# Performance work log

Measured on AMD Instinct MI355X. Metric: run time of the kernel, lower is better.

The kernel has to match this reference:

```python
import jax, jax.numpy as jnp
import numpy as np

BETA = 0.25  # init kwarg; exercises the 0 <= beta < 1 loss branch


def setup_inputs() -> dict:
    key = jax.random.key(0)
    k1, k2 = jax.random.split(key)
    N, D, K = 65536, 64, 4096
    x = jax.random.normal(k1, (N, D), dtype=jnp.float32)
    # original: uniform(-1/K, 1/K) then mean-centered; exact init distribution
    codebook = jax.random.uniform(k2, (K, D), dtype=jnp.float32,
                                  minval=-1.0 / K, maxval=1.0 / K)
    codebook = codebook - codebook.mean(axis=0, keepdims=True)
    return {"x": x, "codebook": codebook}


def reference(x, codebook):
    # pairwise squared distances via sum-of-squares + matmul: [N, K]
    dist = (jnp.sum(x * x, axis=1, keepdims=True)
            + jnp.sum(codebook * codebook, axis=1)
            - 2.0 * jnp.matmul(x, codebook.T))
    encoding_inds = jnp.argmin(dist, axis=1)            # [N]
    # gather codebook rows (equivalent to one-hot @ codebook, no one-hot materialized)
    quantized = jnp.take(codebook, encoding_inds, axis=0)  # [N, D]
    # straight-through estimator
    x_quantized = x + jax.lax.stop_gradient(quantized - x)
    mse = lambda a, b: jnp.mean((a - b) ** 2)
    loss = (BETA * mse(x, jax.lax.stop_gradient(quantized))
            + mse(quantized, jax.lax.stop_gradient(x)))
    return x_quantized, encoding_inds[:, None], loss
```

## Files before the change

kernel.cpp:

```cpp
#include <hip/hip_runtime.h>


#define D  64
#define NT 256

typedef unsigned short u16;
typedef short bf16x8 __attribute__((ext_vector_type(8)));
typedef float f32x4  __attribute__((ext_vector_type(4)));

#define VMWAIT_(n) asm volatile("s_waitcnt vmcnt(" #n ")" ::: "memory")
#define VMWAIT(n) VMWAIT_(n)

__device__ __forceinline__ u16 f32_to_bf16_raw(float f) {
    union { float f; unsigned u; } v; v.f = f;
    unsigned u = v.u;
    u += 0x7FFFu + ((u >> 16) & 1u);
    return (u16)(u >> 16);
}
__device__ __forceinline__ float bf16_raw_to_f32(u16 h) {
    union { unsigned u; float f; } v; v.u = ((unsigned)h) << 16;
    return v.f;
}
__device__ __forceinline__ f32x4 mfma16(bf16x8 a, bf16x8 b, f32x4 c) {
    return __builtin_amdgcn_mfma_f32_16x16x32_bf16(a, b, c, 0, 0, 0);
}

__device__ __forceinline__ float np_pairwise_sumsq_64(const float* p) {
    float r[8];
    #pragma unroll
    for (int j = 0; j < 8; ++j) r[j] = __fmul_rn(p[j], p[j]);
    #pragma unroll
    for (int i = 8; i < 64; i += 8) {
        #pragma unroll
        for (int j = 0; j < 8; ++j)
            r[j] = __fadd_rn(r[j], __fmul_rn(p[i + j], p[i + j]));
    }
    float t0 = __fadd_rn(r[0], r[1]);
    float t1 = __fadd_rn(r[2], r[3]);
    float t2 = __fadd_rn(r[4], r[5]);
    float t3 = __fadd_rn(r[6], r[7]);
    return __fadd_rn(__fadd_rn(t0, t1), __fadd_rn(t2, t3));
}

__global__ __launch_bounds__(256) void prep_kernel(const float* __restrict__ x,
                                                   const float* __restrict__ cb,
                                                   float* __restrict__ sx,
                                                   float* __restrict__ sc,
                                                   bf16x8* __restrict__ cbf,
                                                   int* __restrict__ amb_cnt) {
    int b = blockIdx.x;
    if (b == 0 && threadIdx.x == 0) *amb_cnt = 0;
    if (b < 272) {
        const float* a = (b < 256) ? x : cb;
        float* o = (b < 256) ? sx : sc;
        int r0 = (b < 256) ? b * 256 : (b - 256) * 256;
        int r = r0 + threadIdx.x;
        float buf[64];
        const float4* p = (const float4*)(a + (size_t)r * D);
        #pragma unroll
        for (int i = 0; i < 16; ++i) {
            float4 v = p[i];
            buf[4*i] = v.x; buf[4*i+1] = v.y; buf[4*i+2] = v.z; buf[4*i+3] = v.w;
        }
        o[r] = np_pairwise_sumsq_64(buf);
    } else {
        int t = b - 272;
        int tid = threadIdx.x;
        int lane = tid & 63;
        int ks = (tid >> 6) & 1;
        int hl = tid >> 7;
        int code = t * 16 + (lane & 15);
        int g = lane >> 4;
        bf16x8 v;
        #pragma unroll
        for (int j = 0; j < 8; ++j) {
            int d = ks * 32 + g * 4 + (j & 3) + 16 * (j >> 2);
            float val = cb[(size_t)code * D + d];
            u16 h = f32_to_bf16_raw(val);
            if (hl) {
                float resid = val - bf16_raw_to_f32(h);
                h = f32_to_bf16_raw(resid);
            }
            v[j] = (short)h;
        }
        cbf[((size_t)t * 4 + hl * 2 + ks) * 64 + lane] = v;
    }
}

#define MARG_A 8.0e-6f
#define MARG_B 5.0e-7f

#define STAGE(T, BUF) do {                                                    \
    const char* _src = (const char*)cbf + (size_t)(T) * 4096 + lane * 16;     \
    char* _dst = ringbase + (BUF) * 4096 + lane * 16;                         \
    __builtin_amdgcn_global_load_lds((const __attribute__((address_space(1))) unsigned int*)(_src),        (__attribute__((address_space(3))) unsigned int*)(_dst),        16, 0, 0); \
    __builtin_amdgcn_global_load_lds((const __attribute__((address_space(1))) unsigned int*)(_src + 1024), (__attribute__((address_space(3))) unsigned int*)(_dst + 1024), 16, 0, 0); \
    __builtin_amdgcn_global_load_lds((const __attribute__((address_space(1))) unsigned int*)(_src + 2048), (__attribute__((address_space(3))) unsigned int*)(_dst + 2048), 16, 0, 0); \
    __builtin_amdgcn_global_load_lds((const __attribute__((address_space(1))) unsigned int*)(_src + 3072), (__attribute__((address_space(3))) unsigned int*)(_dst + 3072), 16, 0, 0); \
} while (0)

#define DSREAD(T, BUF, SCK) do {                                              \
    const bf16x8* _bfr = (const bf16x8*)(ringbase + (BUF) * 4096);            \
    Fb0h = _bfr[lane]; Fb1h = _bfr[64 + lane];                                \
    Fb0l = _bfr[128 + lane]; Fb1l = _bfr[192 + lane];                         \
    SCK = scl[(T) * 16 + r];                                                  \
} while (0)

#define MFMAC(P) do {                                                         \
    _Pragma("unroll")                                                         \
    for (int s = 0; s < 4; ++s) {                                             \
        f32x4 _a = {0.f, 0.f, 0.f, 0.f};                                      \
        _a = mfma16(Ah0[s], Fb0h, _a);                                        \
        _a = mfma16(Ah1[s], Fb1h, _a);                                        \
        _a = mfma16(Ah0[s], Fb0l, _a);                                        \
        _a = mfma16(Ah1[s], Fb1l, _a);                                        \
        _a = mfma16(Al0[s], Fb0h, _a);                                        \
        _a = mfma16(Al1[s], Fb1h, _a);                                        \
        P[s] = _a;                                                            \
    }                                                                         \
} while (0)

#define VALUU(P, SCK, T) do {                                                 \
    int _kc = (T) * 16 + r;                                                   \
    _Pragma("unroll")                                                         \
    for (int s = 0; s < 4; ++s) {                                             \
        _Pragma("unroll")                                                     \
        for (int q = 0; q < 4; ++q) {                                         \
            int u = s * 4 + q;                                                \
            float sv = __fmaf_rn(-2.0f, P[s][q], __fadd_rn(sxr[u], SCK));     \
            m2[u] = fminf(m2[u], fmaxf(m1[u], sv));                           \
            bool lt = sv < m1[u];                                             \
            i1[u] = lt ? _kc : i1[u];                                         \
            m1[u] = fminf(m1[u], sv);                                         \
        }                                                                     \
    }                                                                         \
} while (0)

#define ITF(I, BR, BS, PA, PB, SA, SB) do {                                   \
    VMWAIT(4);                                                                \
    DSREAD(t0 + (I) + 2, BR, SB);                                             \
    STAGE(t0 + (I) + 4, BS);                                                  \
    VALUU(PA, SA, t0 + (I));                                                  \
    MFMAC(PB);                                                                \
} while (0)
#define ITN(I, BR, PA, PB, SA, SB, WN) do {                                   \
    VMWAIT(WN);                                                               \
    DSREAD(t0 + (I) + 2, BR, SB);                                             \
    VALUU(PA, SA, t0 + (I));                                                  \
    MFMAC(PB);                                                                \
} while (0)
#define ITV(I, PA, SA) do { VALUU(PA, SA, t0 + (I)); } while (0)

__global__ __launch_bounds__(256, 2) void phase1_kernel(
    const float* __restrict__ x, const float* __restrict__ sx,
    const float* __restrict__ sc, const bf16x8* __restrict__ cbf,
    int* __restrict__ idxbuf, int* __restrict__ amb_cnt, int* __restrict__ amb_rows)
{
    __shared__ __align__(16) char ring[4][3][4096];
    __shared__ float scl[4096];
    __shared__ float lm1[128][2], lm2[128][2];
    __shared__ int   li1[128][2];

    const int tid  = threadIdx.x;
    const int w    = tid >> 6;
    const int lane = tid & 63;
    const int r = lane & 15, g = lane >> 4;
    const int half = w & 1;
    const int rowg = w >> 1;
    const int wbase = blockIdx.x * 128 + rowg * 64;

    for (int j = tid; j < 1024; j += 256)
        *(float4*)&scl[j * 4] = *(const float4*)&sc[j * 4];
    __syncthreads();

    bf16x8 Ah0[4], Ah1[4], Al0[4], Al1[4];
    #pragma unroll
    for (int s = 0; s < 4; ++s) {
        const float* xr = x + (size_t)(wbase + s * 16 + r) * D;
        float e0[8], e1[8];
        float4 f0 = *(const float4*)(xr + g * 4);
        float4 f1 = *(const float4*)(xr + 16 + g * 4);
        float4 f2 = *(const float4*)(xr + 32 + g * 4);
        float4 f3 = *(const float4*)(xr + 48 + g * 4);
        e0[0]=f0.x;e0[1]=f0.y;e0[2]=f0.z;e0[3]=f0.w; e0[4]=f1.x;e0[5]=f1.y;e0[6]=f1.z;e0[7]=f1.w;
        e1[0]=f2.x;e1[1]=f2.y;e1[2]=f2.z;e1[3]=f2.w; e1[4]=f3.x;e1[5]=f3.y;e1[6]=f3.z;e1[7]=f3.w;
        #pragma unroll
        for (int j = 0; j < 8; ++j) {
            u16 h0 = f32_to_bf16_raw(e0[j]);
            Ah0[s][j] = (short)h0;
            Al0[s][j] = (short)f32_to_bf16_raw(e0[j] - bf16_raw_to_f32(h0));
            u16 h1 = f32_to_bf16_raw(e1[j]);
            Ah1[s][j] = (short)h1;
            Al1[s][j] = (short)f32_to_bf16_raw(e1[j] - bf16_raw_to_f32(h1));
        }
    }

    float sxr[16], m1[16], m2[16];
    int   i1[16];
    #pragma unroll
    for (int u = 0; u < 16; ++u) {
        sxr[u] = sx[wbase + (u >> 2) * 16 + g * 4 + (u & 3)];
        m1[u] = 3.4e38f; m2[u] = 3.4e38f; i1[u] = 0;
    }

    const int t0 = half * 128;
    char* ringbase = &ring[w][0][0];

    bf16x8 Fb0h, Fb1h, Fb0l, Fb1l;
    f32x4  P0[4], P1[4], P2[4];
    float  sck0, sck1, sck2;

    VMWAIT(0);
    STAGE(t0 + 0, 0); STAGE(t0 + 1, 1);
    VMWAIT(4); DSREAD(t0 + 0, 0, sck0); STAGE(t0 + 2, 2); MFMAC(P0);
    VMWAIT(4); DSREAD(t0 + 1, 1, sck1); STAGE(t0 + 3, 0); MFMAC(P1);

    #pragma unroll 1
    for (int i = 0; i < 120; i += 3) {
        ITF(i + 0, 2, 1, P0, P2, sck0, sck2);
        ITF(i + 1, 0, 2, P1, P0, sck1, sck0);
        ITF(i + 2, 1, 0, P2, P1, sck2, sck1);
    }
    ITF(120, 2, 1, P0, P2, sck0, sck2);
    ITF(121, 0, 2, P1, P0, sck1, sck0);
    ITF(122, 1, 0, P2, P1, sck2, sck1);
    ITF(123, 2, 1, P0, P2, sck0, sck2);
    ITN(124, 0, P1, P0, sck1, sck0, 4);
    ITN(125, 1, P2, P1, sck2, sck1, 0);
    ITV(126, P0, sck0);
    ITV(127, P1, sck1);

    #pragma unroll
    for (int u = 0; u < 16; ++u) {
        #pragma unroll
        for (int mm = 1; mm < 16; mm <<= 1) {
            float om1 = __shfl_xor(m1[u], mm, 64);
            float om2 = __shfl_xor(m2[u], mm, 64);
            int   oi1 = __shfl_xor(i1[u], mm, 64);
            float nm2 = fminf(fmaxf(m1[u], om1), fminf(m2[u], om2));
            i1[u] = (om1 < m1[u]) ? oi1 : i1[u];
            m1[u] = fminf(m1[u], om1);
            m2[u] = nm2;
        }
    }
    if (r == 0) {
        #pragma unroll
        for (int u = 0; u < 16; ++u) {
            int rowin = rowg * 64 + (u >> 2) * 16 + g * 4 + (u & 3);
            lm1[rowin][half] = m1[u];
            lm2[rowin][half] = m2[u];
            li1[rowin][half] = i1[u];
        }
    }
    __syncthreads();

    if (tid < 128) {
        float a1 = lm1[tid][0], b1 = lm1[tid][1];
        float a2 = lm2[tid][0], b2 = lm2[tid][1];
        int   ia = li1[tid][0], ib = li1[tid][1];
        float m1f = fminf(a1, b1);
        float m2f = fminf(fmaxf(a1, b1), fminf(a2, b2));
        int   i1f = (b1 < a1) ? ib : ia;
        int orow = blockIdx.x * 128 + tid;
        idxbuf[orow] = i1f;
        float marg = __fmaf_rn(sx[orow], MARG_B, MARG_A);
        if (m2f - m1f <= marg) {
            int slot = atomicAdd(amb_cnt, 1);
            amb_rows[slot] = orow;
        }
    }
}

__global__ __launch_bounds__(256) void exact_scan(
    const float* __restrict__ x, const float* __restrict__ cb,
    const float* __restrict__ sx, const float* __restrict__ sc,
    const int* __restrict__ amb_cnt, const int* __restrict__ amb_rows,
    int* __restrict__ idxbuf)
{
    __shared__ float csT[4][64][64];
    __shared__ float xsT[64][16];
    __shared__ float redv[16][64];
    __shared__ int   redi[16][64];
    __shared__ float sxl[16];
    __shared__ int   rowids[16];

    const int tid = threadIdx.x;
    const int cnt = *amb_cnt;
    const int tz = tid >> 6, ty = (tid >> 4) & 3, cx = tid & 15;

    for (int base = blockIdx.x * 16; base < cnt; base += gridDim.x * 16) {
        if (tid < 16) {
            int i = base + tid;
            int rr = (i < cnt) ? amb_rows[i] : amb_rows[base];
            rowids[tid] = rr;
            sxl[tid] = sx[rr];
        }
        __syncthreads();
        {
            int rr = rowids[tid >> 4];
            int dg = tid & 15;
            float4 v = *(const float4*)(x + (size_t)rr * D + dg * 4);
            xsT[dg*4+0][tid>>4] = v.x; xsT[dg*4+1][tid>>4] = v.y;
            xsT[dg*4+2][tid>>4] = v.z; xsT[dg*4+3][tid>>4] = v.w;
        }

        float bv[4]; int bi[4];
        #pragma unroll
        for (int i = 0; i < 4; ++i) { bv[i] = 3.4e38f; bi[i] = 0x7fffffff; }

        for (int st = 0; st < 16; ++st) {
            __syncthreads();
            {
                int code = st * 256 + tid;
                const float4* src = (const float4*)(cb + (size_t)code * D);
                #pragma unroll
                for (int dd = 0; dd < 16; ++dd) {
                    float4 v = src[dd];
                    csT[tid>>6][dd*4+0][tid&63] = v.x; csT[tid>>6][dd*4+1][tid&63] = v.y;
                    csT[tid>>6][dd*4+2][tid&63] = v.z; csT[tid>>6][dd*4+3][tid&63] = v.w;
                }
            }
            __syncthreads();

            float acc[4][4];
            #pragma unroll
            for (int i = 0; i < 4; ++i)
                #pragma unroll
                for (int j = 0; j < 4; ++j) acc[i][j] = 0.0f;

            #pragma unroll 4
            for (int d = 0; d < 64; ++d) {
                float4 xv = *(const float4*)&xsT[d][ty * 4];
                float4 cv = *(const float4*)&csT[tz][d][cx * 4];
                float xr[4] = {xv.x, xv.y, xv.z, xv.w};
                float cc[4] = {cv.x, cv.y, cv.z, cv.w};
                #pragma unroll
                for (int i = 0; i < 4; ++i)
                    #pragma unroll
                    for (int j = 0; j < 4; ++j)
                        acc[i][j] = __fmaf_rn(xr[i], cc[j], acc[i][j]);
            }
            #pragma unroll
            for (int j = 0; j < 4; ++j) {
                int k = st * 256 + tz * 64 + cx * 4 + j;
                float sck = sc[k];
                #pragma unroll
                for (int i = 0; i < 4; ++i) {
                    float tt = __fadd_rn(sxl[ty * 4 + i], sck);
                    float u  = __fmul_rn(2.0f, acc[i][j]);
                    float s  = __fsub_rn(tt, u);
                    if (s < bv[i] || (s == bv[i] && k < bi[i])) { bv[i] = s; bi[i] = k; }
                }
            }
        }

        #pragma unroll
        for (int i = 0; i < 4; ++i) { redv[ty*4+i][tz*16+cx] = bv[i]; redi[ty*4+i][tz*16+cx] = bi[i]; }
        __syncthreads();
        if (tid < 16) {
            float bvv = redv[tid][0]; int bii = redi[tid][0];
            #pragma unroll 8
            for (int i = 1; i < 64; ++i) {
                float v = redv[tid][i]; int k = redi[tid][i];
                if (v < bvv || (v == bvv && k < bii)) { bvv = v; bii = k; }
            }
            idxbuf[rowids[tid]] = bii;
        }
        __syncthreads();
    }
}

__global__ __launch_bounds__(256) void finalize_rows(
    const float* __restrict__ x, const float* __restrict__ cb,
    const int* __restrict__ idxbuf,
    float* __restrict__ out_q, float* __restrict__ out_i,
    double* __restrict__ partials, int N)
{
    __shared__ double wsum[4];
    int wid = threadIdx.x >> 6, lane = threadIdx.x & 63;
    int n = blockIdx.x * 4 + wid;

    int idx = idxbuf[n];
    float q  = cb[(size_t)idx * D + lane];
    float xv = x[(size_t)n * D + lane];
    out_q[(size_t)n * D + lane] = q;

    double diff = (double)xv - (double)q;
    double s = diff * diff;
    #pragma unroll
    for (int off = 32; off > 0; off >>= 1) s += __shfl_down(s, off, 64);
    if (lane == 0) { wsum[wid] = s; out_i[n] = (float)idx; }
    __syncthreads();
    if (threadIdx.x == 0) partials[blockIdx.x] = (wsum[0] + wsum[1]) + (wsum[2] + wsum[3]);
}

__global__ __launch_bounds__(256) void loss_kernel(const double* __restrict__ partials,
                                                   int nP, float* __restrict__ out_loss,
                                                   double invND)
{
    __shared__ double red[256];
    double s = 0.0;
    for (int i = threadIdx.x; i < nP; i += 256) s += partials[i];
    red[threadIdx.x] = s;
    __syncthreads();
    #pragma unroll
    for (int step = 128; step > 0; step >>= 1) {
        if ((int)threadIdx.x < step) red[threadIdx.x] += red[threadIdx.x + step];
        __syncthreads();
    }
    if (threadIdx.x == 0) {
        double m = red[0] * invND;
        out_loss[0] = (float)(0.25 * m + m);
    }
}

extern "C" void kernel_launch(void* const* d_in, const int* in_sizes, int n_in,
                              void* d_out, int out_size, void* d_ws, size_t ws_size,
                              hipStream_t stream)
{
    const float* x  = (const float*)d_in[0];
    const float* cb = (const float*)d_in[1];
    const int N = in_sizes[0] / D;
    const int K = in_sizes[1] / D;

    float* out      = (float*)d_out;
    float* out_q    = out;
    float* out_i    = out + (size_t)N * D;
    float* out_loss = out_i + N;

    char* ws = (char*)d_ws;
    bf16x8* cbf      = (bf16x8*)ws;
    size_t off = (size_t)(K / 16) * 4 * 64 * sizeof(bf16x8);
    float*  sx       = (float*)(ws + off);  off += (size_t)N * 4;
    float*  sc       = (float*)(ws + off);  off += (size_t)K * 4;
    int*    idxbuf   = (int*)(ws + off);    off += (size_t)N * 4;
    int*    amb_rows = (int*)(ws + off);    off += (size_t)N * 4;
    double* partials = (double*)(ws + off); off += (size_t)(N / 4) * 8;
    int*    amb_cnt  = (int*)(ws + off);

    prep_kernel<<<272 + K / 16, 256, 0, stream>>>(x, cb, sx, sc, cbf, amb_cnt);
    phase1_kernel<<<N / 128, 256, 0, stream>>>(x, sx, sc, cbf, idxbuf, amb_cnt, amb_rows);
    exact_scan<<<1024, 256, 0, stream>>>(x, cb, sx, sc, amb_cnt, amb_rows, idxbuf);
    finalize_rows<<<N / 4, 256, 0, stream>>>(x, cb, idxbuf, out_q, out_i, partials, N);
    loss_kernel<<<1, 256, 0, stream>>>(partials, N / 4, out_loss,
                                       1.0 / ((double)N * (double)D));
}
```

Before: 244.3 us.

## Rework phase1 pipeline, drop row-norm term, fuse loss reduction via atomics

The phase1 loop now uses two accumulator sets with a three-slot LDS ring and one-tile lookahead instead of three, and drops the occupancy-2 launch bound. The per-row norm is removed from the inner comparison, since it is constant per row and argmin does not depend on it. The min/second-min update now uses fmed3, and the ambiguity margins are widened to match. The separate loss kernel is replaced by double atomics plus a last-block-done counter inside a grid-strided finalize kernel. This saves a launch and VALU work, but atomics add contention and shallower prefetch may expose latency.

```diff
diff --git a/kernel.cpp b/kernel.cpp
--- a/kernel.cpp
+++ b/kernel.cpp
@@ -47,9 +47,11 @@
                                                    float* __restrict__ sx,
                                                    float* __restrict__ sc,
                                                    bf16x8* __restrict__ cbf,
-                                                   int* __restrict__ amb_cnt) {
+                                                   int* __restrict__ amb_cnt,
+                                                   double* __restrict__ loss_acc,
+                                                   int* __restrict__ done_cnt) {
     int b = blockIdx.x;
-    if (b == 0 && threadIdx.x == 0) *amb_cnt = 0;
+    if (b == 0 && threadIdx.x == 0) { *amb_cnt = 0; *loss_acc = 0.0; *done_cnt = 0; }
     if (b < 272) {
         const float* a = (b < 256) ? x : cb;
         float* o = (b < 256) ? sx : sc;
@@ -87,8 +89,8 @@
     }
 }
 
-#define MARG_A 8.0e-6f
-#define MARG_B 5.0e-7f
+#define MARG_A 1.6e-5f
+#define MARG_B 6.5e-7f
 
 #define STAGE(T, BUF) do {                                                    \
     const char* _src = (const char*)cbf + (size_t)(T) * 4096 + lane * 16;     \
@@ -127,31 +129,24 @@
         _Pragma("unroll")                                                     \
         for (int q = 0; q < 4; ++q) {                                         \
             int u = s * 4 + q;                                                \
-            float sv = __fmaf_rn(-2.0f, P[s][q], __fadd_rn(sxr[u], SCK));     \
-            m2[u] = fminf(m2[u], fmaxf(m1[u], sv));                           \
-            bool lt = sv < m1[u];                                             \
-            i1[u] = lt ? _kc : i1[u];                                         \
-            m1[u] = fminf(m1[u], sv);                                         \
+            float sv = __fmaf_rn(-2.0f, P[s][q], SCK);                        \
+            float m1o = m1[u];                                                \
+            m2[u] = __builtin_amdgcn_fmed3f(sv, m1o, m2[u]);                  \
+            i1[u] = (sv < m1o) ? _kc : i1[u];                                 \
+            m1[u] = fminf(m1o, sv);                                           \
         }                                                                     \
     }                                                                         \
 } while (0)
 
-#define ITF(I, BR, BS, PA, PB, SA, SB) do {                                   \
+#define ITX(I, Pv, Sv, Pm, Sm, BR, BS) do {                                   \
     VMWAIT(4);                                                                \
-    DSREAD(t0 + (I) + 2, BR, SB);                                             \
-    STAGE(t0 + (I) + 4, BS);                                                  \
-    VALUU(PA, SA, t0 + (I));                                                  \
-    MFMAC(PB);                                                                \
+    DSREAD(t0 + (I) + 1, BR, Sm);                                             \
+    STAGE(t0 + (I) + 3, BS);                                                  \
+    VALUU(Pv, Sv, t0 + (I));                                                  \
+    MFMAC(Pm);                                                                \
 } while (0)
-#define ITN(I, BR, PA, PB, SA, SB, WN) do {                                   \
-    VMWAIT(WN);                                                               \
-    DSREAD(t0 + (I) + 2, BR, SB);                                             \
-    VALUU(PA, SA, t0 + (I));                                                  \
-    MFMAC(PB);                                                                \
-} while (0)
-#define ITV(I, PA, SA) do { VALUU(PA, SA, t0 + (I)); } while (0)
-
-__global__ __launch_bounds__(256, 2) void phase1_kernel(
+
+__global__ __launch_bounds__(256) void phase1_kernel(
     const float* __restrict__ x, const float* __restrict__ sx,
     const float* __restrict__ sc, const bf16x8* __restrict__ cbf,
     int* __restrict__ idxbuf, int* __restrict__ amb_cnt, int* __restrict__ amb_rows)
@@ -195,40 +190,41 @@
         }
     }
 
-    float sxr[16], m1[16], m2[16];
+    float m1[16], m2[16];
     int   i1[16];
     #pragma unroll
-    for (int u = 0; u < 16; ++u) {
-        sxr[u] = sx[wbase + (u >> 2) * 16 + g * 4 + (u & 3)];
-        m1[u] = 3.4e38f; m2[u] = 3.4e38f; i1[u] = 0;
-    }
+    for (int u = 0; u < 16; ++u) { m1[u] = 3.4e38f; m2[u] = 3.4e38f; i1[u] = 0; }
 
     const int t0 = half * 128;
     char* ringbase = &ring[w][0][0];
 
     bf16x8 Fb0h, Fb1h, Fb0l, Fb1l;
-    f32x4  P0[4], P1[4], P2[4];
-    float  sck0, sck1, sck2;
+    f32x4  PA[4], PB[4];
+    float  sA, sB;
 
     VMWAIT(0);
-    STAGE(t0 + 0, 0); STAGE(t0 + 1, 1);
-    VMWAIT(4); DSREAD(t0 + 0, 0, sck0); STAGE(t0 + 2, 2); MFMAC(P0);
-    VMWAIT(4); DSREAD(t0 + 1, 1, sck1); STAGE(t0 + 3, 0); MFMAC(P1);
+    STAGE(t0 + 0, 0); STAGE(t0 + 1, 1); STAGE(t0 + 2, 2);
+    VMWAIT(8);
+    DSREAD(t0 + 0, 0, sA);
+    MFMAC(PA);
 
     #pragma unroll 1
-    for (int i = 0; i < 120; i += 3) {
-        ITF(i + 0, 2, 1, P0, P2, sck0, sck2);
-        ITF(i + 1, 0, 2, P1, P0, sck1, sck0);
-        ITF(i + 2, 1, 0, P2, P1, sck2, sck1);
-    }
-    ITF(120, 2, 1, P0, P2, sck0, sck2);
-    ITF(121, 0, 2, P1, P0, sck1, sck0);
-    ITF(122, 1, 0, P2, P1, sck2, sck1);
-    ITF(123, 2, 1, P0, P2, sck0, sck2);
-    ITN(124, 0, P1, P0, sck1, sck0, 4);
-    ITN(125, 1, P2, P1, sck2, sck1, 0);
-    ITV(126, P0, sck0);
-    ITV(127, P1, sck1);
+    for (int i = 0; i < 120; i += 6) {
+        ITX(i + 0, PA, sA, PB, sB, 1, 0);
+        ITX(i + 1, PB, sB, PA, sA, 2, 1);
+        ITX(i + 2, PA, sA, PB, sB, 0, 2);
+        ITX(i + 3, PB, sB, PA, sA, 1, 0);
+        ITX(i + 4, PA, sA, PB, sB, 2, 1);
+        ITX(i + 5, PB, sB, PA, sA, 0, 2);
+    }
+    ITX(120, PA, sA, PB, sB, 1, 0);
+    ITX(121, PB, sB, PA, sA, 2, 1);
+    ITX(122, PA, sA, PB, sB, 0, 2);
+    ITX(123, PB, sB, PA, sA, 1, 0);
+    ITX(124, PA, sA, PB, sB, 2, 1);
+    VMWAIT(4); DSREAD(t0 + 126, 0, sA); VALUU(PB, sB, t0 + 125); MFMAC(PA);
+    VMWAIT(0); DSREAD(t0 + 127, 1, sB); VALUU(PA, sA, t0 + 126); MFMAC(PB);
+    VALUU(PB, sB, t0 + 127);
 
     #pragma unroll
     for (int u = 0; u < 16; ++u) {
@@ -374,43 +370,40 @@
     const float* __restrict__ x, const float* __restrict__ cb,
     const int* __restrict__ idxbuf,
     float* __restrict__ out_q, float* __restrict__ out_i,
-    double* __restrict__ partials, int N)
+    double* __restrict__ loss_acc, int* __restrict__ done_cnt,
+    float* __restrict__ out_loss, int N)
 {
     __shared__ double wsum[4];
     int wid = threadIdx.x >> 6, lane = threadIdx.x & 63;
-    int n = blockIdx.x * 4 + wid;
-
-    int idx = idxbuf[n];
-    float q  = cb[(size_t)idx * D + lane];
-    float xv = x[(size_t)n * D + lane];
-    out_q[(size_t)n * D + lane] = q;
-
-    double diff = (double)xv - (double)q;
-    double s = diff * diff;
-    #pragma unroll
-    for (int off = 32; off > 0; off >>= 1) s += __shfl_down(s, off, 64);
-    if (lane == 0) { wsum[wid] = s; out_i[n] = (float)idx; }
-    __syncthreads();
-    if (threadIdx.x == 0) partials[blockIdx.x] = (wsum[0] + wsum[1]) + (wsum[2] + wsum[3]);
-}
-
-__global__ __launch_bounds__(256) void loss_kernel(const double* __restrict__ partials,
-                                                   int nP, float* __restrict__ out_loss,
-                                                   double invND)
-{
-    __shared__ double red[256];
-    double s = 0.0;
-    for (int i = threadIdx.x; i < nP; i += 256) s += partials[i];
-    red[threadIdx.x] = s;
-    __syncthreads();
-    #pragma unroll
-    for (int step = 128; step > 0; step >>= 1) {
-        if ((int)threadIdx.x < step) red[threadIdx.x] += red[threadIdx.x + step];
+    const int nchunks = N / 4;
+
+    for (int chunk = blockIdx.x; chunk < nchunks; chunk += gridDim.x) {
+        int n = chunk * 4 + wid;
+
+        int idx = idxbuf[n];
+        float q  = cb[(size_t)idx * D + lane];
+        float xv = x[(size_t)n * D + lane];
+        out_q[(size_t)n * D + lane] = q;
+
+        double diff = (double)xv - (double)q;
+        double s = diff * diff;
+        #pragma unroll
+        for (int off = 32; off > 0; off >>= 1) s += __shfl_down(s, off, 64);
+        if (lane == 0) { wsum[wid] = s; out_i[n] = (float)idx; }
         __syncthreads();
-    }
-    if (threadIdx.x == 0) {
-        double m = red[0] * invND;
-        out_loss[0] = (float)(0.25 * m + m);
+        if (threadIdx.x == 0) {
+            double part = (wsum[0] + wsum[1]) + (wsum[2] + wsum[3]);
+            atomicAdd(loss_acc, part);
+            __threadfence();
+            int done = atomicAdd(done_cnt, 1);
+            if (done == nchunks - 1) {
+                __threadfence();
+                double tot = atomicAdd(loss_acc, 0.0);
+                double m = tot / ((double)N * (double)D);
+                out_loss[0] = (float)(0.25 * m + m);
+            }
+        }
+        __syncthreads();
     }
 }
 
@@ -435,13 +428,14 @@
     float*  sc       = (float*)(ws + off);  off += (size_t)K * 4;
     int*    idxbuf   = (int*)(ws + off);    off += (size_t)N * 4;
     int*    amb_rows = (int*)(ws + off);    off += (size_t)N * 4;
-    double* partials = (double*)(ws + off); off += (size_t)(N / 4) * 8;
-    int*    amb_cnt  = (int*)(ws + off);
-
-    prep_kernel<<<272 + K / 16, 256, 0, stream>>>(x, cb, sx, sc, cbf, amb_cnt);
+    double* loss_acc = (double*)(ws + off); off += 8;
+    int*    amb_cnt  = (int*)(ws + off);    off += 4;
+    int*    done_cnt = (int*)(ws + off);
+
+    prep_kernel<<<272 + K / 16, 256, 0, stream>>>(x, cb, sx, sc, cbf,
+                                                  amb_cnt, loss_acc, done_cnt);
     phase1_kernel<<<N / 128, 256, 0, stream>>>(x, sx, sc, cbf, idxbuf, amb_cnt, amb_rows);
     exact_scan<<<1024, 256, 0, stream>>>(x, cb, sx, sc, amb_cnt, amb_rows, idxbuf);
-    finalize_rows<<<N / 4, 256, 0, stream>>>(x, cb, idxbuf, out_q, out_i, partials, N);
-    loss_kernel<<<1, 256, 0, stream>>>(partials, N / 4, out_loss,
-                                       1.0 / ((double)N * (double)D));
-}
+    finalize_rows<<<2048, 256, 0, stream>>>(x, cb, idxbuf, out_q, out_i,
+                                            loss_acc, done_cnt, out_loss, N);
+}
```

After: 624.5 us. +155.6%, slower.
